# Kernel optimization log

Measured on AMD Instinct MI355X. Metric: run time of the kernel, lower is better.

## Reference

```python
import jax, jax.numpy as jnp
import numpy as np

B, S, D = 4, 2048, 1024   # batch, seq_len, d_model
H, DK, DV = 16, 64, 64    # heads, key_size, head_size
NEG_BIG = 1e12


def setup_inputs() -> dict:
    key = jax.random.key(0)
    ks = jax.random.split(key, 11)
    s = 0.02  # weight scale
    return {
        "q": jax.random.normal(ks[0], (B, S, D), jnp.float32),
        "k": jax.random.normal(ks[1], (B, S, D), jnp.float32),
        "v": jax.random.normal(ks[2], (B, S, D), jnp.float32),
        "q_mask": jnp.ones((B, S), jnp.int32),
        "v_mask": jnp.ones((B, S), jnp.int32),
        "Wq": jax.random.normal(ks[3], (D, H * DK), jnp.float32) * s,
        "bq": jnp.zeros((H * DK,), jnp.float32),
        "Wk": jax.random.normal(ks[4], (D, H * DK), jnp.float32) * s,
        "bk": jnp.zeros((H * DK,), jnp.float32),
        "Wv": jax.random.normal(ks[5], (D, H * DV), jnp.float32) * s,
        "bv": jnp.zeros((H * DV,), jnp.float32),
        "Wo": jax.random.normal(ks[6], (H * DV, H * DV), jnp.float32) * s,
        "bo": jnp.zeros((H * DV,), jnp.float32),
    }


def reference(q, k, v, q_mask, v_mask, Wq, bq, Wk, bk, Wv, bv, Wo, bo):
    Bq, Sq, _ = q.shape
    Sk = k.shape[1]
    # projections -> (B, S, H, d)
    qw = (q @ Wq + bq).reshape(Bq, Sq, H, DK)
    kw = (k @ Wk + bk).reshape(Bq, Sk, H, DK)
    vw = (v @ Wv + bv).reshape(Bq, Sk, H, DV)
    # scores: (B, H, Sq, Sk)
    a = jnp.einsum('bjhd,bkhd->bhjk', qw, kw) / jnp.asarray(DK, qw.dtype) ** 0.5
    # v_mask: additive -inf-style masking on key axis (mode=1, axis=-1)
    vm = v_mask.astype(a.dtype)[:, None, None, :]
    a = a - (1.0 - vm) * NEG_BIG
    # a_mask = 'history_only' causal mask
    causal = jnp.tril(jnp.ones((Sq, Sk), a.dtype))
    a = a - (1.0 - causal) * NEG_BIG
    a = jax.nn.softmax(a, axis=-1)
    # attention output: (B, Sq, H, DV) -> (B, Sq, H*DV)
    o = jnp.einsum('bhjk,bkhd->bjhd', a, vw).reshape(Bq, Sq, H * DV)
    o = o @ Wo + bo
    # q_mask: multiplicative zeroing of padded query rows (mode=0)
    o = o * q_mask.astype(o.dtype)[:, :, None]
    return o
```

## Files before the change

kernel.cpp:

```cpp
#include <hip/hip_runtime.h>
#include <hip/hip_bf16.h>

#define Bb 4
#define Ss 2048
#define Dm 1024
#define Hh 16
#define DKk 64
#define DVv 64

using short8  = __attribute__((ext_vector_type(8))) short;
using short4v = __attribute__((ext_vector_type(4))) short;
using floatx4 = __attribute__((ext_vector_type(4))) float;

__device__ inline unsigned short f32_to_bf16(float f) {
    union { float f; unsigned int u; } x; x.f = f;
    unsigned int r = x.u + 0x7fffu + ((x.u >> 16) & 1u);
    return (unsigned short)(r >> 16);
}

__device__ inline unsigned int cvt_pk_bf16(float a, float b) {
    unsigned int r;
    asm("v_cvt_pk_bf16_f32 %0, %1, %2" : "=v"(r) : "v"(a), "v"(b));
    return r;
}

__device__ inline void dma16(const unsigned short* g, unsigned short* l) {
    __builtin_amdgcn_global_load_lds(
        (const __attribute__((address_space(1))) void*)g,
        (__attribute__((address_space(3))) void*)l, 16, 0, 0);
}

__global__ __launch_bounds__(256) void transpose_w4(
        const float* __restrict__ W0, const float* __restrict__ W1,
        const float* __restrict__ W2, const float* __restrict__ W3,
        unsigned short* __restrict__ T0, unsigned short* __restrict__ T1,
        unsigned short* __restrict__ T2, unsigned short* __restrict__ T3) {
    const float* W; unsigned short* Wt;
    switch (blockIdx.z) {
        case 0: W = W0; Wt = T0; break;
        case 1: W = W1; Wt = T1; break;
        case 2: W = W2; Wt = T2; break;
        default: W = W3; Wt = T3; break;
    }
    __shared__ float tile[32][33];
    int n0 = blockIdx.x * 32, k0 = blockIdx.y * 32;
    int tx = threadIdx.x, ty = threadIdx.y;
    #pragma unroll
    for (int i = 0; i < 32; i += 8)
        tile[ty + i][tx] = W[(size_t)(k0 + ty + i) * Dm + n0 + tx];
    __syncthreads();
    #pragma unroll
    for (int i = 0; i < 32; i += 8)
        Wt[(size_t)(n0 + ty + i) * Dm + k0 + tx] = f32_to_bf16(tile[tx][ty + i]);
}

__global__ __launch_bounds__(256) void gemm_proj_f32(
        const float* __restrict__ Aq, const float* __restrict__ Ak,
        const float* __restrict__ Av,
        const unsigned short* __restrict__ Btq, const unsigned short* __restrict__ Btk,
        const unsigned short* __restrict__ Btv,
        const float* __restrict__ bq, const float* __restrict__ bk,
        const float* __restrict__ bv,
        unsigned short* __restrict__ Oq, unsigned short* __restrict__ Ok,
        unsigned short* __restrict__ Ov) {
    const float* A; const unsigned short* Bt; const float* bias;
    unsigned short* Out; int mode;
    switch (blockIdx.z) {
        case 0:  A = Aq; Bt = Btq; bias = bq; Out = Oq; mode = 0; break;
        case 1:  A = Ak; Bt = Btk; bias = bk; Out = Ok; mode = 0; break;
        default: A = Av; Bt = Btv; bias = bv; Out = Ov; mode = 1; break;
    }
    const int wave = threadIdx.x >> 6;
    const int lane = threadIdx.x & 63;
    const int quad = lane >> 4;
    const int l16  = lane & 15;
    const int wr = wave & 1, wc = wave >> 1;
    const int m0 = blockIdx.x * 128;
    const int n0 = blockIdx.y * 128;

    __shared__ __align__(16) unsigned short Alds[2][4096];
    __shared__ __align__(16) unsigned short Blds[2][4096];

    const float* Asrc[2];
    const unsigned short* Bsrc[2];
    int Adst[2], Bdst[2];
    #pragma unroll
    for (int i = 0; i < 2; i++) {
        int L = (wave * 2 + i) * 64 + lane;
        int row = L >> 2, cpr = L & 3;
        int csrc = cpr ^ ((row >> 1) & 3);
        Adst[i] = L * 8;
        Bdst[i] = (wave * 2 + i) * 512;
        Asrc[i] = A  + (size_t)(m0 + row) * Dm + csrc * 8;
        Bsrc[i] = Bt + (size_t)(n0 + row) * Dm + csrc * 8;
    }

    int aoff[4], boff[4];
    #pragma unroll
    for (int r = 0; r < 4; r++) {
        int row = wr * 64 + r * 16 + l16;
        aoff[r] = row * 32 + (quad ^ ((row >> 1) & 3)) * 8;
        row = wc * 64 + r * 16 + l16;
        boff[r] = row * 32 + (quad ^ ((row >> 1) & 3)) * 8;
    }

    float4 ar[2][2];
    #pragma unroll
    for (int i = 0; i < 2; i++) {
        ar[i][0] = *(const float4*)(Asrc[i]);
        ar[i][1] = *(const float4*)(Asrc[i] + 4);
    }
    #pragma unroll
    for (int i = 0; i < 2; i++) {
        dma16(Bsrc[i], &Blds[0][Bdst[i]]);
        union { short8 v; unsigned int u[4]; } w;
        w.u[0] = cvt_pk_bf16(ar[i][0].x, ar[i][0].y);
        w.u[1] = cvt_pk_bf16(ar[i][0].z, ar[i][0].w);
        w.u[2] = cvt_pk_bf16(ar[i][1].x, ar[i][1].y);
        w.u[3] = cvt_pk_bf16(ar[i][1].z, ar[i][1].w);
        *(short8*)(&Alds[0][Adst[i]]) = w.v;
        ar[i][0] = *(const float4*)(Asrc[i] + 32);
        ar[i][1] = *(const float4*)(Asrc[i] + 36);
    }
    __syncthreads();

    floatx4 acc[4][4] = {};
    int cur = 0;

    for (int k0 = 0; k0 < Dm; k0 += 32) {
        if (k0 + 32 < Dm) {
            #pragma unroll
            for (int i = 0; i < 2; i++) {
                dma16(Bsrc[i] + k0 + 32, &Blds[cur ^ 1][Bdst[i]]);
                union { short8 v; unsigned int u[4]; } w;
                w.u[0] = cvt_pk_bf16(ar[i][0].x, ar[i][0].y);
                w.u[1] = cvt_pk_bf16(ar[i][0].z, ar[i][0].w);
                w.u[2] = cvt_pk_bf16(ar[i][1].x, ar[i][1].y);
                w.u[3] = cvt_pk_bf16(ar[i][1].z, ar[i][1].w);
                *(short8*)(&Alds[cur ^ 1][Adst[i]]) = w.v;
            }
            if (k0 + 64 < Dm) {
                #pragma unroll
                for (int i = 0; i < 2; i++) {
                    ar[i][0] = *(const float4*)(Asrc[i] + k0 + 64);
                    ar[i][1] = *(const float4*)(Asrc[i] + k0 + 68);
                }
            }
        }

        short8 a[4], b[4];
        #pragma unroll
        for (int r = 0; r < 4; r++) a[r] = *(const short8*)(&Alds[cur][0] + aoff[r]);
        #pragma unroll
        for (int c = 0; c < 4; c++) b[c] = *(const short8*)(&Blds[cur][0] + boff[c]);
        #pragma unroll
        for (int r = 0; r < 4; r++)
            #pragma unroll
            for (int c = 0; c < 4; c++)
                acc[r][c] = __builtin_amdgcn_mfma_f32_16x16x32_bf16(a[r], b[c], acc[r][c], 0, 0, 0);

        __syncthreads();
        cur ^= 1;
    }

    #pragma unroll
    for (int r = 0; r < 4; r++)
        #pragma unroll
        for (int c = 0; c < 4; c++) {
            int n = n0 + wc * 64 + c * 16 + l16;
            float bias_n = bias[n];
            int h = n >> 6, d = n & 63;
            #pragma unroll
            for (int i = 0; i < 4; i++) {
                int m = m0 + wr * 64 + r * 16 + quad * 4 + i;
                unsigned short ob = f32_to_bf16(acc[r][c][i] + bias_n);
                int bb = m >> 11, s = m & (Ss - 1);
                if (mode == 0)
                    Out[((size_t)(bb * Hh + h) * Ss + s) * 64 + d] = ob;
                else
                    Out[(((size_t)(bb * Hh + h) * 32 + (s >> 6)) * 64 + d) * 64 + (s & 63)] = ob;
            }
        }
}

__global__ __launch_bounds__(256) void gemm_final(const unsigned short* __restrict__ A,
                                                  const unsigned short* __restrict__ Bt,
                                                  const float* __restrict__ bias,
                                                  const int* __restrict__ q_mask,
                                                  float* __restrict__ Out) {
    const int wave = threadIdx.x >> 6;
    const int lane = threadIdx.x & 63;
    const int quad = lane >> 4;
    const int l16  = lane & 15;
    const int wr = wave & 1, wc = wave >> 1;
    const int m0 = blockIdx.x * 128;
    const int n0 = blockIdx.y * 128;

    __shared__ __align__(16) unsigned short Alds[2][4096];
    __shared__ __align__(16) unsigned short Blds[2][4096];

    const unsigned short* Asrc[2];
    const unsigned short* Bsrc[2];
    int Ldst[2];
    #pragma unroll
    for (int i = 0; i < 2; i++) {
        int L = (wave * 2 + i) * 64 + lane;
        int row = L >> 2, cpr = L & 3;
        int csrc = cpr ^ ((row >> 1) & 3);
        Ldst[i] = (wave * 2 + i) * 512;
        Asrc[i] = A  + (size_t)(m0 + row) * Dm + csrc * 8;
        Bsrc[i] = Bt + (size_t)(n0 + row) * Dm + csrc * 8;
    }

    int aoff[4], boff[4];
    #pragma unroll
    for (int r = 0; r < 4; r++) {
        int row = wr * 64 + r * 16 + l16;
        aoff[r] = row * 32 + (quad ^ ((row >> 1) & 3)) * 8;
        row = wc * 64 + r * 16 + l16;
        boff[r] = row * 32 + (quad ^ ((row >> 1) & 3)) * 8;
    }

    #pragma unroll
    for (int i = 0; i < 2; i++) {
        dma16(Asrc[i], &Alds[0][Ldst[i]]);
        dma16(Bsrc[i], &Blds[0][Ldst[i]]);
    }
    __syncthreads();

    floatx4 acc[4][4] = {};
    int cur = 0;

    for (int k0 = 0; k0 < Dm; k0 += 32) {
        if (k0 + 32 < Dm) {
            #pragma unroll
            for (int i = 0; i < 2; i++) {
                dma16(Asrc[i] + k0 + 32, &Alds[cur ^ 1][Ldst[i]]);
                dma16(Bsrc[i] + k0 + 32, &Blds[cur ^ 1][Ldst[i]]);
            }
        }

        short8 a[4], b[4];
        #pragma unroll
        for (int r = 0; r < 4; r++) a[r] = *(const short8*)(&Alds[cur][0] + aoff[r]);
        #pragma unroll
        for (int c = 0; c < 4; c++) b[c] = *(const short8*)(&Blds[cur][0] + boff[c]);
        #pragma unroll
        for (int r = 0; r < 4; r++)
            #pragma unroll
            for (int c = 0; c < 4; c++)
                acc[r][c] = __builtin_amdgcn_mfma_f32_16x16x32_bf16(a[r], b[c], acc[r][c], 0, 0, 0);

        __syncthreads();
        cur ^= 1;
    }

    #pragma unroll
    for (int r = 0; r < 4; r++)
        #pragma unroll
        for (int c = 0; c < 4; c++) {
            int n = n0 + wc * 64 + c * 16 + l16;
            float bias_n = bias[n];
            #pragma unroll
            for (int i = 0; i < 4; i++) {
                int m = m0 + wr * 64 + r * 16 + quad * 4 + i;
                float qm = (float)q_mask[m];
                Out[(size_t)m * Dm + n] = (acc[r][c][i] + bias_n) * qm;
            }
        }
}

#define SCL 0.18033688f
#define PEN 1.44269504e12f

__global__ __launch_bounds__(256, 2) void attn_kernel(const unsigned short* __restrict__ Qp,
                                                      const unsigned short* __restrict__ Kp,
                                                      const unsigned short* __restrict__ Vt,
                                                      const int* __restrict__ v_mask,
                                                      unsigned short* __restrict__ AO) {
    const int tid  = threadIdx.x;
    const int wave = tid >> 6;
    const int lane = tid & 63;
    const int quad = lane >> 4;
    const int l16  = lane & 15;

    const int n   = blockIdx.x;
    const int hi4 = n >> 8, lo = n & 255;
    const int t2  = (lo >> 6) & 3;
    const int h   = (lo & 63) >> 2;
    const int b   = lo & 3;
    int qt;
    switch (hi4) {
        case 0:  qt = t2;      break;
        case 1:  qt = 15 - t2; break;
        case 2:  qt = 7 - t2;  break;
        default: qt = 8 + t2;  break;
    }
    const int bh = b * Hh + h;

    __shared__ __align__(16) unsigned short Klds[2][4096];
    __shared__ __align__(16) unsigned short Vlds[2][4096];
    __shared__ int allv[32];

    {
        const int tile = tid >> 3, sub = tid & 7;
        const int4 vmA = *(const int4*)(v_mask + b * Ss + tile * 64 + sub * 8);
        const int4 vmB = *(const int4*)(v_mask + b * Ss + tile * 64 + sub * 8 + 4);
        const bool ok = vmA.x && vmA.y && vmA.z && vmA.w &&
                        vmB.x && vmB.y && vmB.z && vmB.w;
        const unsigned long long bal = __ballot(ok);
        if (sub == 0)
            allv[tile] = (int)(((bal >> ((tile & 7) * 8)) & 0xFFull) == 0xFFull);
    }

    int srcOff[2], ldsDst[2];
    #pragma unroll
    for (int i = 0; i < 2; i++) {
        int G = i * 256 + tid;
        int grow = G >> 3, gc = G & 7;
        int fS = (grow & 3) | ((grow >> 1) & 4);
        srcOff[i] = grow * 64 + (gc ^ fS) * 8;
        ldsDst[i] = i * 2048 + wave * 512;
    }
    const unsigned short* Kt_base = Kp + (size_t)bh * Ss * 64;
    const unsigned short* Vt_base = Vt + (size_t)bh * 32 * 4096;
    const int* vm_base = v_mask + b * Ss;

    const int l3 = l16 & 3;
    const int fK = l3 | (((l16 >> 2) & 1) << 2);
    const int kslot = (quad ^ fK) * 8;
    int koff[4];
    #pragma unroll
    for (int kf = 0; kf < 4; kf++) {
        int row = (kf & 1) * 32 + ((l16 >> 2) << 3) + ((kf >> 1) << 2) + l3;
        koff[kf] = row * 64 + kslot;
    }
    const int fV = l3 | (((l16 >> 3) & 1) << 2);
    const int vslot = (quad ^ fV) * 8;
    int voff[4];
    #pragma unroll
    for (int f = 0; f < 4; f++) voff[f] = (f * 16 + l16) * 64 + vslot;

    short8 ones;
    #pragma unroll
    for (int i = 0; i < 8; i++) ones[i] = (short)0x3F80;

    const int kbq = quad * 8;

    const int qbase = qt * 128 + wave * 32;
    const int q0 = qbase + l16;
    const unsigned short* qptr = Qp + ((size_t)bh * Ss + q0) * 64 + quad * 8;
    const short8 qf0 = *(const short8*)(qptr);
    const short8 qf1 = *(const short8*)(qptr + 32);
    const short8 qg0 = *(const short8*)(qptr + 16 * 64);
    const short8 qg1 = *(const short8*)(qptr + 16 * 64 + 32);

    floatx4 o0[4] = {}, o1[4] = {};
    floatx4 sm0 = {}, sm1 = {};

    const int diagw = 2 * qt + (wave >> 1);
    const int KT    = 2 * qt + 2;

    #pragma unroll
    for (int i = 0; i < 2; i++) {
        dma16(Kt_base + srcOff[i], &Klds[0][ldsDst[i]]);
        dma16(Vt_base + srcOff[i], &Vlds[0][ldsDst[i]]);
    }
    __syncthreads();

    int cur = 0;
    for (int kt = 0; kt < KT; kt++) {
        if (kt + 1 < KT) {
            const unsigned short* kn = Kt_base + (size_t)(kt + 1) * 4096;
            const unsigned short* vn = Vt_base + (size_t)(kt + 1) * 4096;
            #pragma unroll
            for (int i = 0; i < 2; i++) {
                dma16(kn + srcOff[i], &Klds[cur ^ 1][ldsDst[i]]);
                dma16(vn + srcOff[i], &Vlds[cur ^ 1][ldsDst[i]]);
            }
        }

        if (kt <= diagw) {
            const unsigned short* Kc = &Klds[cur][0];
            const unsigned short* Vc = &Vlds[cur][0];
            const int kk = kt * 64;

            floatx4 st0[4], st1[4];
            #pragma unroll
            for (int kf = 0; kf < 4; kf++) {
                short8 a0 = *(const short8*)(Kc + koff[kf]);
                short8 a1 = *(const short8*)(Kc + (koff[kf] ^ 32));
                floatx4 t = {};
                t = __builtin_amdgcn_mfma_f32_16x16x32_bf16(a0, qf0, t, 0, 0, 0);
                t = __builtin_amdgcn_mfma_f32_16x16x32_bf16(a1, qf1, t, 0, 0, 0);
                st0[kf] = t;
                floatx4 u = {};
                u = __builtin_amdgcn_mfma_f32_16x16x32_bf16(a0, qg0, u, 0, 0, 0);
                u = __builtin_amdgcn_mfma_f32_16x16x32_bf16(a1, qg1, u, 0, 0, 0);
                st1[kf] = u;
            }

            unsigned int pk0[4][2], pk1[4][2];
            if ((kt == diagw) || (!allv[kt])) {
                #pragma unroll
                for (int kf = 0; kf < 4; kf++) {
                    const int kb = kk + (kf & 1) * 32 + kbq + ((kf >> 1) << 2);
                    const int4 vm = *(const int4*)(vm_base + kb);
                    const int vmi[4] = {vm.x, vm.y, vm.z, vm.w};
                    float p0[4], p1[4];
                    #pragma unroll
                    for (int i = 0; i < 4; i++) {
                        const int key = kb + i;
                        const float penm = (vmi[i] == 0) ? PEN : 0.f;
                        const float pe0 = penm + ((key > q0) ? PEN : 0.f);
                        const float pe1 = penm + ((key > q0 + 16) ? PEN : 0.f);
                        p0[i] = exp2f(fmaf(st0[kf][i], SCL, -pe0));
                        p1[i] = exp2f(fmaf(st1[kf][i], SCL, -pe1));
                    }
                    pk0[kf][0] = cvt_pk_bf16(p0[0], p0[1]);
                    pk0[kf][1] = cvt_pk_bf16(p0[2], p0[3]);
                    pk1[kf][0] = cvt_pk_bf16(p1[0], p1[1]);
                    pk1[kf][1] = cvt_pk_bf16(p1[2], p1[3]);
                }
            } else {
                #pragma unroll
                for (int kf = 0; kf < 4; kf++) {
                    float p0[4], p1[4];
                    #pragma unroll
                    for (int i = 0; i < 4; i++) {
                        p0[i] = exp2f(st0[kf][i] * SCL);
                        p1[i] = exp2f(st1[kf][i] * SCL);
                    }
                    pk0[kf][0] = cvt_pk_bf16(p0[0], p0[1]);
                    pk0[kf][1] = cvt_pk_bf16(p0[2], p0[3]);
                    pk1[kf][0] = cvt_pk_bf16(p1[0], p1[1]);
                    pk1[kf][1] = cvt_pk_bf16(p1[2], p1[3]);
                }
            }

            union { short8 s; unsigned int u[4]; } pA0, pA1, pB0, pB1;
            pA0.u[0] = pk0[0][0]; pA0.u[1] = pk0[0][1];
            pA0.u[2] = pk0[2][0]; pA0.u[3] = pk0[2][1];
            pA1.u[0] = pk0[1][0]; pA1.u[1] = pk0[1][1];
            pA1.u[2] = pk0[3][0]; pA1.u[3] = pk0[3][1];
            pB0.u[0] = pk1[0][0]; pB0.u[1] = pk1[0][1];
            pB0.u[2] = pk1[2][0]; pB0.u[3] = pk1[2][1];
            pB1.u[0] = pk1[1][0]; pB1.u[1] = pk1[1][1];
            pB1.u[2] = pk1[3][0]; pB1.u[3] = pk1[3][1];

            sm0 = __builtin_amdgcn_mfma_f32_16x16x32_bf16(ones, pA0.s, sm0, 0, 0, 0);
            sm0 = __builtin_amdgcn_mfma_f32_16x16x32_bf16(ones, pA1.s, sm0, 0, 0, 0);
            sm1 = __builtin_amdgcn_mfma_f32_16x16x32_bf16(ones, pB0.s, sm1, 0, 0, 0);
            sm1 = __builtin_amdgcn_mfma_f32_16x16x32_bf16(ones, pB1.s, sm1, 0, 0, 0);

            #pragma unroll
            for (int f = 0; f < 4; f++) {
                short8 v0 = *(const short8*)(Vc + voff[f]);
                short8 v1 = *(const short8*)(Vc + (voff[f] ^ 32));
                o0[f] = __builtin_amdgcn_mfma_f32_16x16x32_bf16(v0, pA0.s, o0[f], 0, 0, 0);
                o0[f] = __builtin_amdgcn_mfma_f32_16x16x32_bf16(v1, pA1.s, o0[f], 0, 0, 0);
                o1[f] = __builtin_amdgcn_mfma_f32_16x16x32_bf16(v0, pB0.s, o1[f], 0, 0, 0);
                o1[f] = __builtin_amdgcn_mfma_f32_16x16x32_bf16(v1, pB1.s, o1[f], 0, 0, 0);
            }
        }

        __syncthreads();
        cur ^= 1;
    }

    const float ri0 = 1.0f / sm0[0];
    const float ri1 = 1.0f / sm1[0];
    unsigned short* aop0 = AO + ((size_t)b * Ss + q0) * (Hh * DVv) + h * 64 + quad * 4;
    unsigned short* aop1 = aop0 + (size_t)16 * (Hh * DVv);
    #pragma unroll
    for (int f = 0; f < 4; f++) {
        int2 w0, w1;
        w0.x = (int)cvt_pk_bf16(o0[f][0] * ri0, o0[f][1] * ri0);
        w0.y = (int)cvt_pk_bf16(o0[f][2] * ri0, o0[f][3] * ri0);
        *(int2*)(aop0 + f * 16) = w0;
        w1.x = (int)cvt_pk_bf16(o1[f][0] * ri1, o1[f][1] * ri1);
        w1.y = (int)cvt_pk_bf16(o1[f][2] * ri1, o1[f][3] * ri1);
        *(int2*)(aop1 + f * 16) = w1;
    }
}

extern "C" void kernel_launch(void* const* d_in, const int* in_sizes, int n_in,
                              void* d_out, int out_size, void* d_ws, size_t ws_size,
                              hipStream_t stream) {
    const float* q      = (const float*)d_in[0];
    const float* k      = (const float*)d_in[1];
    const float* v      = (const float*)d_in[2];
    const int*   q_mask = (const int*)d_in[3];
    const int*   v_mask = (const int*)d_in[4];
    const float* Wq     = (const float*)d_in[5];
    const float* bq     = (const float*)d_in[6];
    const float* Wk     = (const float*)d_in[7];
    const float* bk     = (const float*)d_in[8];
    const float* Wv     = (const float*)d_in[9];
    const float* bv     = (const float*)d_in[10];
    const float* Wo     = (const float*)d_in[11];
    const float* bo     = (const float*)d_in[12];
    float* out = (float*)d_out;

    char* ws = (char*)d_ws;
    const size_t WT_SZ = (size_t)Dm * Dm * 2;
    const size_t QP_SZ = (size_t)Bb * Hh * Ss * 64 * 2;
    unsigned short* Wtq = (unsigned short*)(ws);
    unsigned short* Wtk = (unsigned short*)(ws + WT_SZ);
    unsigned short* Wtv = (unsigned short*)(ws + 2 * WT_SZ);
    unsigned short* Wto = (unsigned short*)(ws + 3 * WT_SZ);
    unsigned short* Qp  = (unsigned short*)(ws + 4 * WT_SZ);
    unsigned short* Kp  = (unsigned short*)(ws + 4 * WT_SZ + QP_SZ);
    unsigned short* Vt  = (unsigned short*)(ws + 4 * WT_SZ + 2 * QP_SZ);
    unsigned short* AO  = (unsigned short*)(ws + 4 * WT_SZ + 3 * QP_SZ);

    hipLaunchKernelGGL(transpose_w4, dim3(Dm / 32, Dm / 32, 4), dim3(32, 8), 0, stream,
                       Wq, Wk, Wv, Wo, Wtq, Wtk, Wtv, Wto);

    const int M = Bb * Ss;
    dim3 gp(M / 128, Dm / 128, 3);
    hipLaunchKernelGGL(gemm_proj_f32, gp, dim3(256), 0, stream,
                       q, k, v, Wtq, Wtk, Wtv, bq, bk, bv, Qp, Kp, Vt);

    dim3 ag(Bb * Hh * (Ss / 128), 1, 1);
    hipLaunchKernelGGL(attn_kernel, ag, dim3(256), 0, stream, Qp, Kp, Vt, v_mask, AO);

    dim3 gg(M / 128, Dm / 128);
    hipLaunchKernelGGL(gemm_final, gg, dim3(256), 0, stream, AO, Wto, bo, q_mask, out);
}
```

Before: 348.8 us.

## Enlarge GEMM block tiles to 256x256 and 256x128 with 512-thread blocks

The projection GEMM moves from 128x128 tiles with 4 waves to 256x256 tiles with 8 waves, each wave computing a 128x64 sub-tile. The output GEMM moves to 256x128 tiles with 8 waves, each computing 128x32. Larger tiles reuse each loaded A/B element across more MFMAs, which cuts global and LDS traffic per flop. In exchange they use more registers and LDS per block, and the projection grid becomes 32x4x3=384 blocks, which may not fully occupy the GPU's CUs.

```diff
diff --git a/kernel.cpp b/kernel.cpp
--- a/kernel.cpp
+++ b/kernel.cpp
@@ -54,7 +54,7 @@
         Wt[(size_t)(n0 + ty + i) * Dm + k0 + tx] = f32_to_bf16(tile[tx][ty + i]);
 }
 
-__global__ __launch_bounds__(256) void gemm_proj_f32(
+__global__ __launch_bounds__(512) void gemm_proj_f32(
         const float* __restrict__ Aq, const float* __restrict__ Ak,
         const float* __restrict__ Av,
         const unsigned short* __restrict__ Btq, const unsigned short* __restrict__ Btk,
@@ -70,38 +70,42 @@
         case 1:  A = Ak; Bt = Btk; bias = bk; Out = Ok; mode = 0; break;
         default: A = Av; Bt = Btv; bias = bv; Out = Ov; mode = 1; break;
     }
-    const int wave = threadIdx.x >> 6;
-    const int lane = threadIdx.x & 63;
+    const int tid  = threadIdx.x;
+    const int wave = tid >> 6;
+    const int lane = tid & 63;
     const int quad = lane >> 4;
     const int l16  = lane & 15;
-    const int wr = wave & 1, wc = wave >> 1;
-    const int m0 = blockIdx.x * 128;
-    const int n0 = blockIdx.y * 128;
-
-    __shared__ __align__(16) unsigned short Alds[2][4096];
-    __shared__ __align__(16) unsigned short Blds[2][4096];
+    const int wr = wave >> 2, wc = wave & 3;
+    const int m0 = blockIdx.x * 256;
+    const int n0 = blockIdx.y * 256;
+
+    __shared__ __align__(16) unsigned short Alds[2][8192];
+    __shared__ __align__(16) unsigned short Blds[2][8192];
 
     const float* Asrc[2];
     const unsigned short* Bsrc[2];
     int Adst[2], Bdst[2];
     #pragma unroll
     for (int i = 0; i < 2; i++) {
-        int L = (wave * 2 + i) * 64 + lane;
+        int L = i * 512 + tid;
         int row = L >> 2, cpr = L & 3;
         int csrc = cpr ^ ((row >> 1) & 3);
         Adst[i] = L * 8;
-        Bdst[i] = (wave * 2 + i) * 512;
+        Bdst[i] = (i * 512 + wave * 64) * 8;
         Asrc[i] = A  + (size_t)(m0 + row) * Dm + csrc * 8;
         Bsrc[i] = Bt + (size_t)(n0 + row) * Dm + csrc * 8;
     }
 
-    int aoff[4], boff[4];
-    #pragma unroll
-    for (int r = 0; r < 4; r++) {
-        int row = wr * 64 + r * 16 + l16;
+    int aoff[8], boff[4];
+    #pragma unroll
+    for (int r = 0; r < 8; r++) {
+        int row = wr * 128 + r * 16 + l16;
         aoff[r] = row * 32 + (quad ^ ((row >> 1) & 3)) * 8;
-        row = wc * 64 + r * 16 + l16;
-        boff[r] = row * 32 + (quad ^ ((row >> 1) & 3)) * 8;
+    }
+    #pragma unroll
+    for (int c = 0; c < 4; c++) {
+        int row = wc * 64 + c * 16 + l16;
+        boff[c] = row * 32 + (quad ^ ((row >> 1) & 3)) * 8;
     }
 
     float4 ar[2][2];
@@ -111,8 +115,10 @@
         ar[i][1] = *(const float4*)(Asrc[i] + 4);
     }
     #pragma unroll
+    for (int i = 0; i < 2; i++)
+        dma16(Bsrc[i], &Blds[0][Bdst[i]]);
+    #pragma unroll
     for (int i = 0; i < 2; i++) {
-        dma16(Bsrc[i], &Blds[0][Bdst[i]]);
         union { short8 v; unsigned int u[4]; } w;
         w.u[0] = cvt_pk_bf16(ar[i][0].x, ar[i][0].y);
         w.u[1] = cvt_pk_bf16(ar[i][0].z, ar[i][0].w);
@@ -124,14 +130,16 @@
     }
     __syncthreads();
 
-    floatx4 acc[4][4] = {};
+    floatx4 acc[8][4] = {};
     int cur = 0;
 
     for (int k0 = 0; k0 < Dm; k0 += 32) {
         if (k0 + 32 < Dm) {
             #pragma unroll
+            for (int i = 0; i < 2; i++)
+                dma16(Bsrc[i] + k0 + 32, &Blds[cur ^ 1][Bdst[i]]);
+            #pragma unroll
             for (int i = 0; i < 2; i++) {
-                dma16(Bsrc[i] + k0 + 32, &Blds[cur ^ 1][Bdst[i]]);
                 union { short8 v; unsigned int u[4]; } w;
                 w.u[0] = cvt_pk_bf16(ar[i][0].x, ar[i][0].y);
                 w.u[1] = cvt_pk_bf16(ar[i][0].z, ar[i][0].w);
@@ -148,13 +156,13 @@
             }
         }
 
-        short8 a[4], b[4];
-        #pragma unroll
-        for (int r = 0; r < 4; r++) a[r] = *(const short8*)(&Alds[cur][0] + aoff[r]);
+        short8 a[8], b[4];
+        #pragma unroll
+        for (int r = 0; r < 8; r++) a[r] = *(const short8*)(&Alds[cur][0] + aoff[r]);
         #pragma unroll
         for (int c = 0; c < 4; c++) b[c] = *(const short8*)(&Blds[cur][0] + boff[c]);
         #pragma unroll
-        for (int r = 0; r < 4; r++)
+        for (int r = 0; r < 8; r++)
             #pragma unroll
             for (int c = 0; c < 4; c++)
                 acc[r][c] = __builtin_amdgcn_mfma_f32_16x16x32_bf16(a[r], b[c], acc[r][c], 0, 0, 0);
@@ -164,7 +172,7 @@
     }
 
     #pragma unroll
-    for (int r = 0; r < 4; r++)
+    for (int r = 0; r < 8; r++)
         #pragma unroll
         for (int c = 0; c < 4; c++) {
             int n = n0 + wc * 64 + c * 16 + l16;
@@ -172,7 +180,7 @@
             int h = n >> 6, d = n & 63;
             #pragma unroll
             for (int i = 0; i < 4; i++) {
-                int m = m0 + wr * 64 + r * 16 + quad * 4 + i;
+                int m = m0 + wr * 128 + r * 16 + quad * 4 + i;
                 unsigned short ob = f32_to_bf16(acc[r][c][i] + bias_n);
                 int bb = m >> 11, s = m & (Ss - 1);
                 if (mode == 0)
@@ -183,72 +191,80 @@
         }
 }
 
-__global__ __launch_bounds__(256) void gemm_final(const unsigned short* __restrict__ A,
+__global__ __launch_bounds__(512) void gemm_final(const unsigned short* __restrict__ A,
                                                   const unsigned short* __restrict__ Bt,
                                                   const float* __restrict__ bias,
                                                   const int* __restrict__ q_mask,
                                                   float* __restrict__ Out) {
-    const int wave = threadIdx.x >> 6;
-    const int lane = threadIdx.x & 63;
+    const int tid  = threadIdx.x;
+    const int wave = tid >> 6;
+    const int lane = tid & 63;
     const int quad = lane >> 4;
     const int l16  = lane & 15;
-    const int wr = wave & 1, wc = wave >> 1;
-    const int m0 = blockIdx.x * 128;
+    const int wr = wave >> 2, wc = wave & 3;
+    const int m0 = blockIdx.x * 256;
     const int n0 = blockIdx.y * 128;
 
-    __shared__ __align__(16) unsigned short Alds[2][4096];
+    __shared__ __align__(16) unsigned short Alds[2][8192];
     __shared__ __align__(16) unsigned short Blds[2][4096];
 
     const unsigned short* Asrc[2];
-    const unsigned short* Bsrc[2];
-    int Ldst[2];
+    const unsigned short* Bsrc;
+    int Adst[2], Bdst;
     #pragma unroll
     for (int i = 0; i < 2; i++) {
-        int L = (wave * 2 + i) * 64 + lane;
+        int L = i * 512 + tid;
         int row = L >> 2, cpr = L & 3;
         int csrc = cpr ^ ((row >> 1) & 3);
-        Ldst[i] = (wave * 2 + i) * 512;
-        Asrc[i] = A  + (size_t)(m0 + row) * Dm + csrc * 8;
-        Bsrc[i] = Bt + (size_t)(n0 + row) * Dm + csrc * 8;
-    }
-
-    int aoff[4], boff[4];
-    #pragma unroll
-    for (int r = 0; r < 4; r++) {
-        int row = wr * 64 + r * 16 + l16;
+        Adst[i] = (i * 512 + wave * 64) * 8;
+        Asrc[i] = A + (size_t)(m0 + row) * Dm + csrc * 8;
+    }
+    {
+        int L = tid;
+        int row = L >> 2, cpr = L & 3;
+        int csrc = cpr ^ ((row >> 1) & 3);
+        Bdst = wave * 64 * 8;
+        Bsrc = Bt + (size_t)(n0 + row) * Dm + csrc * 8;
+    }
+
+    int aoff[8], boff[2];
+    #pragma unroll
+    for (int r = 0; r < 8; r++) {
+        int row = wr * 128 + r * 16 + l16;
         aoff[r] = row * 32 + (quad ^ ((row >> 1) & 3)) * 8;
-        row = wc * 64 + r * 16 + l16;
-        boff[r] = row * 32 + (quad ^ ((row >> 1) & 3)) * 8;
-    }
-
-    #pragma unroll
-    for (int i = 0; i < 2; i++) {
-        dma16(Asrc[i], &Alds[0][Ldst[i]]);
-        dma16(Bsrc[i], &Blds[0][Ldst[i]]);
-    }
+    }
+    #pragma unroll
+    for (int c = 0; c < 2; c++) {
+        int row = wc * 32 + c * 16 + l16;
+        boff[c] = row * 32 + (quad ^ ((row >> 1) & 3)) * 8;
+    }
+
+    #pragma unroll
+    for (int i = 0; i < 2; i++)
+        dma16(Asrc[i], &Alds[0][Adst[i]]);
+    dma16(Bsrc, &Blds[0][Bdst]);
     __syncthreads();
 
-    floatx4 acc[4][4] = {};
+    floatx4 acc[8][2] = {};
     int cur = 0;
 
     for (int k0 = 0; k0 < Dm; k0 += 32) {
         if (k0 + 32 < Dm) {
             #pragma unroll
-            for (int i = 0; i < 2; i++) {
-                dma16(Asrc[i] + k0 + 32, &Alds[cur ^ 1][Ldst[i]]);
-                dma16(Bsrc[i] + k0 + 32, &Blds[cur ^ 1][Ldst[i]]);
-            }
+            for (int i = 0; i < 2; i++)
+                dma16(Asrc[i] + k0 + 32, &Alds[cur ^ 1][Adst[i]]);
+            dma16(Bsrc + k0 + 32, &Blds[cur ^ 1][Bdst]);
         }
 
-        short8 a[4], b[4];
-        #pragma unroll
-        for (int r = 0; r < 4; r++) a[r] = *(const short8*)(&Alds[cur][0] + aoff[r]);
-        #pragma unroll
-        for (int c = 0; c < 4; c++) b[c] = *(const short8*)(&Blds[cur][0] + boff[c]);
-        #pragma unroll
-        for (int r = 0; r < 4; r++)
-            #pragma unroll
-            for (int c = 0; c < 4; c++)
+        short8 a[8], b[2];
+        #pragma unroll
+        for (int r = 0; r < 8; r++) a[r] = *(const short8*)(&Alds[cur][0] + aoff[r]);
+        #pragma unroll
+        for (int c = 0; c < 2; c++) b[c] = *(const short8*)(&Blds[cur][0] + boff[c]);
+        #pragma unroll
+        for (int r = 0; r < 8; r++)
+            #pragma unroll
+            for (int c = 0; c < 2; c++)
                 acc[r][c] = __builtin_amdgcn_mfma_f32_16x16x32_bf16(a[r], b[c], acc[r][c], 0, 0, 0);
 
         __syncthreads();
@@ -256,14 +272,14 @@
     }
 
     #pragma unroll
-    for (int r = 0; r < 4; r++)
-        #pragma unroll
-        for (int c = 0; c < 4; c++) {
-            int n = n0 + wc * 64 + c * 16 + l16;
+    for (int r = 0; r < 8; r++)
+        #pragma unroll
+        for (int c = 0; c < 2; c++) {
+            int n = n0 + wc * 32 + c * 16 + l16;
             float bias_n = bias[n];
             #pragma unroll
             for (int i = 0; i < 4; i++) {
-                int m = m0 + wr * 64 + r * 16 + quad * 4 + i;
+                int m = m0 + wr * 128 + r * 16 + quad * 4 + i;
                 float qm = (float)q_mask[m];
                 Out[(size_t)m * Dm + n] = (acc[r][c][i] + bias_n) * qm;
             }
@@ -518,13 +534,13 @@
                        Wq, Wk, Wv, Wo, Wtq, Wtk, Wtv, Wto);
 
     const int M = Bb * Ss;
-    dim3 gp(M / 128, Dm / 128, 3);
-    hipLaunchKernelGGL(gemm_proj_f32, gp, dim3(256), 0, stream,
+    dim3 gp(M / 256, Dm / 256, 3);
+    hipLaunchKernelGGL(gemm_proj_f32, gp, dim3(512), 0, stream,
                        q, k, v, Wtq, Wtk, Wtv, bq, bk, bv, Qp, Kp, Vt);
 
     dim3 ag(Bb * Hh * (Ss / 128), 1, 1);
     hipLaunchKernelGGL(attn_kernel, ag, dim3(256), 0, stream, Qp, Kp, Vt, v_mask, AO);
 
-    dim3 gg(M / 128, Dm / 128);
-    hipLaunchKernelGGL(gemm_final, gg, dim3(256), 0, stream, AO, Wto, bo, q_mask, out);
-}
+    dim3 gg(M / 256, Dm / 128);
+    hipLaunchKernelGGL(gemm_final, gg, dim3(512), 0, stream, AO, Wto, bo, q_mask, out);
+}
```

Result: slower. 385.7 us (+10.6%).
